# Performance work log

Measured on AMD Instinct MI355X. Metric: run time of the kernel, lower is better.

Reference implementation:

```python
import jax, jax.numpy as jnp
import numpy as np

N_NODES = 50000
N_EDGES = 400000
IN_CH = 165
HID = 64
HEADS = 8
EPS = 1e-5
NEG_SLOPE = 0.2


def _layer_norm(x, g, b):
    mu = jnp.mean(x, axis=-1, keepdims=True)
    var = jnp.mean(jnp.square(x - mu), axis=-1, keepdims=True)
    return (x - mu) * jax.lax.rsqrt(var + EPS) * g + b


def _gat_conv(x, src, dst, W, a_src, a_dst, bias, concat):
    # x: [N, F_in]; src/dst: [E] (self-loops already appended)
    N = x.shape[0]
    H, C = a_src.shape
    h = (x @ W).reshape(N, H, C)                       # [N, H, C]
    alpha_s = jnp.sum(h * a_src, axis=-1)              # [N, H]
    alpha_d = jnp.sum(h * a_dst, axis=-1)              # [N, H]
    e = jax.nn.leaky_relu(alpha_s[src] + alpha_d[dst], NEG_SLOPE)  # [E, H]
    # segment softmax over incoming edges of each dst node
    m = jax.ops.segment_max(e, dst, num_segments=N)    # [N, H]
    m = jnp.where(jnp.isfinite(m), m, 0.0)
    ex = jnp.exp(e - m[dst])                           # [E, H]
    denom = jax.ops.segment_sum(ex, dst, num_segments=N)  # [N, H]
    alpha = ex / denom[dst]                            # [E, H]
    out = jax.ops.segment_sum(alpha[:, :, None] * h[src], dst, num_segments=N)  # [N, H, C]
    if concat:
        out = out.reshape(N, H * C)
    else:
        out = out.mean(axis=1)
    return out + bias


def setup_inputs() -> dict:
    key = jax.random.key(0)
    ks = jax.random.split(key, 24)
    sc = 0.05
    d = {
        'x': jax.random.normal(ks[0], (N_NODES, IN_CH), dtype=jnp.float32),
        'edge_index': jax.random.randint(ks[1], (2, N_EDGES), 0, N_NODES, dtype=jnp.int64),
        # layer 0: in=165 -> heads*hid=512 (concat)
        'W0': jax.random.normal(ks[2], (IN_CH, HEADS * HID), jnp.float32) * sc,
        'as0': jax.random.normal(ks[3], (HEADS, HID), jnp.float32) * sc,
        'ad0': jax.random.normal(ks[4], (HEADS, HID), jnp.float32) * sc,
        'b0': jnp.zeros((HEADS * HID,), jnp.float32),
        'lng0': jnp.ones((HEADS * HID,), jnp.float32),
        'lnb0': jnp.zeros((HEADS * HID,), jnp.float32),
        # layer 1: 512 -> 512 (concat, residual applies)
        'W1': jax.random.normal(ks[5], (HEADS * HID, HEADS * HID), jnp.float32) * sc,
        'as1': jax.random.normal(ks[6], (HEADS, HID), jnp.float32) * sc,
        'ad1': jax.random.normal(ks[7], (HEADS, HID), jnp.float32) * sc,
        'b1': jnp.zeros((HEADS * HID,), jnp.float32),
        'lng1': jnp.ones((HEADS * HID,), jnp.float32),
        'lnb1': jnp.zeros((HEADS * HID,), jnp.float32),
        # layer 2: 512 -> 64 (mean over heads)
        'W2': jax.random.normal(ks[8], (HEADS * HID, HEADS * HID), jnp.float32) * sc,
        'as2': jax.random.normal(ks[9], (HEADS, HID), jnp.float32) * sc,
        'ad2': jax.random.normal(ks[10], (HEADS, HID), jnp.float32) * sc,
        'b2': jnp.zeros((HID,), jnp.float32),
        'lng2': jnp.ones((HID,), jnp.float32),
        'lnb2': jnp.zeros((HID,), jnp.float32),
        'lin_w': jax.random.normal(ks[11], (HID, 2), jnp.float32) * sc,
        'lin_b': jnp.zeros((2,), jnp.float32),
    }
    return d


def reference(x, edge_index, W0, as0, ad0, b0, lng0, lnb0,
              W1, as1, ad1, b1, lng1, lnb1,
              W2, as2, ad2, b2, lng2, lnb2, lin_w, lin_b):
    N = x.shape[0]
    loops = jnp.arange(N, dtype=edge_index.dtype)
    src = jnp.concatenate([edge_index[0], loops])
    dst = jnp.concatenate([edge_index[1], loops])

    layers = [
        (W0, as0, ad0, b0, lng0, lnb0, True),
        (W1, as1, ad1, b1, lng1, lnb1, True),
        (W2, as2, ad2, b2, lng2, lnb2, False),
    ]
    h = x
    for (W, a_s, a_d, b, g, bb, concat) in layers:
        residual = h
        h = _gat_conv(h, src, dst, W, a_s, a_d, b, concat)
        if h.shape == residual.shape:
            h = h + residual
        h = _layer_norm(h, g, bb)
        h = jax.nn.relu(h)
        # dropout is identity in eval mode
    return h @ lin_w + lin_b
```

## Files before the change

### kernel.cpp

```cpp
#include <hip/hip_runtime.h>
#include <hip/hip_bf16.h>
#include <cstdint>
#include <cstddef>

#define HEADS 8
#define HID 64
#define HF 512
#define NEG_SLOPE 0.2f
#define LN_EPS 1e-5f

typedef __hip_bfloat16 bf16;
typedef __attribute__((ext_vector_type(8))) __bf16 bf16v8;
typedef __attribute__((ext_vector_type(4))) float f32x4;

__device__ __forceinline__ float wsum64(float v) {
#pragma unroll
  for (int o = 32; o > 0; o >>= 1) v += __shfl_xor(v, o, 64);
  return v;
}
__device__ __forceinline__ int wsum64i(int v) {
#pragma unroll
  for (int o = 32; o > 0; o >>= 1) v += __shfl_xor(v, o, 64);
  return v;
}
__device__ __forceinline__ float leaky(float v) { return v >= 0.f ? v : NEG_SLOPE * v; }
__device__ __forceinline__ float bits2f(unsigned short u) {
  return __uint_as_float(((unsigned)u) << 16);
}
__device__ __forceinline__ unsigned short f2bits(float x) {
  union { bf16 h; unsigned short u; } bu;
  bu.h = __float2bfloat16(x);
  return bu.u;
}

__global__ __launch_bounds__(256)
void convert_count(const int* __restrict__ ei, int* __restrict__ esrc,
                   int* __restrict__ edst, int* __restrict__ counts, int E) {
  int e = blockIdx.x * 256 + threadIdx.x;
  if (e >= E) return;
  bool i64 = (ei[1] == 0) && (ei[3] == 0) && (ei[5] == 0) && (ei[7] == 0);
  int s, d;
  if (i64) { s = ei[2 * (size_t)e]; d = ei[2 * ((size_t)E + e)]; }
  else     { s = ei[e];             d = ei[E + e]; }
  esrc[e] = s; edst[e] = d;
  atomicAdd(&counts[d], 1);
}

#define SCAN_T 256
#define SCAN_EPT 4
#define SCAN_CHUNK (SCAN_T * SCAN_EPT)

__global__ __launch_bounds__(SCAN_T)
void scan_pass1(const int* __restrict__ counts, int* __restrict__ bsum, int N) {
  int b = blockIdx.x, t = threadIdx.x;
  int base = b * SCAN_CHUNK + t * SCAN_EPT;
  int s = 0;
#pragma unroll
  for (int i = 0; i < SCAN_EPT; ++i) {
    int idx = base + i;
    if (idx < N) s += counts[idx] + 1;
  }
  int lane = t & 63, w = t >> 6;
  int tot = wsum64i(s);
  __shared__ int ws[4];
  if (lane == 0) ws[w] = tot;
  __syncthreads();
  if (t == 0) bsum[b] = ws[0] + ws[1] + ws[2] + ws[3];
}

__global__ __launch_bounds__(64)
void scan_pass2(const int* __restrict__ bsum, int* __restrict__ boff, int NB) {
  int t = threadIdx.x;
  int own = t < NB ? bsum[t] : 0;
  int v = own;
#pragma unroll
  for (int o = 1; o < 64; o <<= 1) {
    int u = __shfl_up(v, o, 64);
    if (t >= o) v += u;
  }
  if (t < NB) boff[t] = v - own;
}

__global__ __launch_bounds__(SCAN_T)
void scan_pass3(const int* __restrict__ counts, const int* __restrict__ boff,
                int* __restrict__ row_ptr, int* __restrict__ cursor, int N, int Etot) {
  int b = blockIdx.x, t = threadIdx.x;
  int base = b * SCAN_CHUNK + t * SCAN_EPT;
  int c[SCAN_EPT];
  int s = 0;
#pragma unroll
  for (int i = 0; i < SCAN_EPT; ++i) {
    int idx = base + i;
    c[i] = idx < N ? counts[idx] + 1 : 0;
    s += c[i];
  }
  int lane = t & 63, w = t >> 6;
  int inc = s;
#pragma unroll
  for (int o = 1; o < 64; o <<= 1) {
    int u = __shfl_up(inc, o, 64);
    if (lane >= o) inc += u;
  }
  __shared__ int wsums[4];
  if (lane == 63) wsums[w] = inc;
  __syncthreads();
  int woff = 0;
  for (int i = 0; i < w; ++i) woff += wsums[i];
  int run = inc - s + woff + boff[b];
#pragma unroll
  for (int i = 0; i < SCAN_EPT; ++i) {
    int idx = base + i;
    if (idx < N) { row_ptr[idx] = run; cursor[idx] = run; run += c[i]; }
  }
  if (b == 0 && t == 0) row_ptr[N] = Etot;
}

__global__ __launch_bounds__(256)
void scatter_kernel(const int* __restrict__ esrc, const int* __restrict__ edst,
                    int* __restrict__ cursor, int* __restrict__ col, int N, int E) {
  int e = blockIdx.x * 256 + threadIdx.x;
  int Etot = E + N;
  if (e >= Etot) return;
  int s = e < E ? esrc[e] : e - E;
  int d = e < E ? edst[e] : e - E;
  int pos = atomicAdd(&cursor[d], 1);
  col[pos] = s;
}

__global__ __launch_bounds__(256)
void convert_pad_x(const float* __restrict__ x, bf16* __restrict__ xbf,
                   int M, int K, int Kp) {
  int idx = blockIdx.x * 256 + threadIdx.x;
  if (idx >= M * Kp) return;
  int row = idx / Kp, colk = idx - row * Kp;
  float v = colk < K ? x[(size_t)row * K + colk] : 0.f;
  xbf[idx] = __float2bfloat16(v);
}

__global__ __launch_bounds__(256)
void transpose_w(const float* __restrict__ W, bf16* __restrict__ Wt,
                 int K, int Ncols, int Kp) {
  int idx = blockIdx.x * 256 + threadIdx.x;
  if (idx >= Ncols * Kp) return;
  int n = idx / Kp, k = idx - n * Kp;
  float v = k < K ? W[(size_t)k * Ncols + n] : 0.f;
  Wt[idx] = __float2bfloat16(v);
}

#define LDSW 40
__global__ __launch_bounds__(256)
void gemm_mfma(const bf16* __restrict__ A, const bf16* __restrict__ Bt,
               bf16* __restrict__ C,
               const float* __restrict__ as_g, const float* __restrict__ ad_g,
               float* __restrict__ alpha_s, float* __restrict__ alpha_d,
               int M, int Ncols, int K) {
  __shared__ short Alds[128 * LDSW];
  __shared__ short Blds[128 * LDSW];
  const int tid = threadIdx.x;
  const int wave = tid >> 6, lane = tid & 63;
  const int wr = wave >> 1, wc = wave & 1;
  const int row0 = blockIdx.x * 128, col0 = blockIdx.y * 128;
  const int lrow = lane & 15;
  const int kc = lane >> 4;
  f32x4 acc[4][4] = {};

  for (int k0 = 0; k0 < K; k0 += 32) {
#pragma unroll
    for (int i = 0; i < 2; ++i) {
      int idx = tid + i * 256;
      int r = idx >> 2, c4 = idx & 3;
      uint4 va = make_uint4(0, 0, 0, 0);
      int gm = row0 + r;
      if (gm < M) va = *reinterpret_cast<const uint4*>(A + (size_t)gm * K + k0 + c4 * 8);
      *reinterpret_cast<uint4*>(&Alds[r * LDSW + c4 * 8]) = va;
      uint4 vb = *reinterpret_cast<const uint4*>(Bt + (size_t)(col0 + r) * K + k0 + c4 * 8);
      *reinterpret_cast<uint4*>(&Blds[r * LDSW + c4 * 8]) = vb;
    }
    __syncthreads();
    bf16v8 af[4], bfr[4];
#pragma unroll
    for (int r = 0; r < 4; ++r)
      af[r] = *reinterpret_cast<const bf16v8*>(&Alds[(wr * 64 + r * 16 + lrow) * LDSW + kc * 8]);
#pragma unroll
    for (int c = 0; c < 4; ++c)
      bfr[c] = *reinterpret_cast<const bf16v8*>(&Blds[(wc * 64 + c * 16 + lrow) * LDSW + kc * 8]);
#pragma unroll
    for (int r = 0; r < 4; ++r)
#pragma unroll
      for (int c = 0; c < 4; ++c)
        acc[r][c] = __builtin_amdgcn_mfma_f32_16x16x32_bf16(af[r], bfr[c], acc[r][c], 0, 0, 0);
    __syncthreads();
  }

  const int crow = (lane >> 4) * 4;
  const int ccol = lane & 15;
#pragma unroll
  for (int r = 0; r < 4; ++r) {
#pragma unroll
    for (int c = 0; c < 4; ++c) {
      int gc = col0 + wc * 64 + c * 16 + ccol;
#pragma unroll
      for (int j = 0; j < 4; ++j) {
        int gr = row0 + wr * 64 + r * 16 + crow + j;
        if (gr < M) C[(size_t)gr * Ncols + gc] = __float2bfloat16(acc[r][c][j]);
      }
    }
  }

  const int head = (col0 + wc * 64) >> 6;
  float asf[4], adf[4];
#pragma unroll
  for (int c = 0; c < 4; ++c) {
    asf[c] = as_g[head * HID + c * 16 + ccol];
    adf[c] = ad_g[head * HID + c * 16 + ccol];
  }
#pragma unroll
  for (int r = 0; r < 4; ++r) {
#pragma unroll
    for (int j = 0; j < 4; ++j) {
      float ps = 0.f, pd = 0.f;
#pragma unroll
      for (int c = 0; c < 4; ++c) {
        ps = fmaf(acc[r][c][j], asf[c], ps);
        pd = fmaf(acc[r][c][j], adf[c], pd);
      }
#pragma unroll
      for (int o = 1; o < 16; o <<= 1) {
        ps += __shfl_xor(ps, o, 64);
        pd += __shfl_xor(pd, o, 64);
      }
      if (ccol == 0) {
        int gr = row0 + wr * 64 + r * 16 + crow + j;
        if (gr < M) {
          alpha_s[gr * HEADS + head] = ps;
          alpha_d[gr * HEADS + head] = pd;
        }
      }
    }
  }
}

template <int LAYER>
__global__ __launch_bounds__(256)
void aggregate_kernel(const int* __restrict__ row_ptr, const int* __restrict__ col,
                      const bf16* __restrict__ hbuf,
                      const float* __restrict__ alpha_s, const float* __restrict__ alpha_d,
                      const bf16* __restrict__ resid,
                      const float* __restrict__ bias, const float* __restrict__ g,
                      const float* __restrict__ b,
                      bf16* __restrict__ out_bf, int N) {
  int w = threadIdx.x >> 6;
  int lane = threadIdx.x & 63;
  int nn = blockIdx.x * 4 + w;
  bool valid = nn < N;
  int n = valid ? nn : 0;
  int h = lane >> 3;
  float adh = alpha_d[n * HEADS + h];
  float m = -1e30f, den = 0.f;
  float a[8] = {};
  int lo = row_ptr[n], hi = row_ptr[n + 1];

  int sj = col[lo];
  float asj = alpha_s[sj * HEADS + h];
  uint4 u = *reinterpret_cast<const uint4*>(hbuf + (size_t)sj * HF + lane * 8);

  for (int j = lo; j < hi; ++j) {
    float e = leaky(asj + adh);
    uint4 uc = u;
    if (j + 1 < hi) {
      int sn = col[j + 1];
      asj = alpha_s[sn * HEADS + h];
      u = *reinterpret_cast<const uint4*>(hbuf + (size_t)sn * HF + lane * 8);
    }
    if (e > m) {
      float sc = __expf(m - e);
      den *= sc;
#pragma unroll
      for (int i = 0; i < 8; ++i) a[i] *= sc;
      m = e;
    }
    float ex = __expf(e - m);
    den += ex;
    const unsigned short* us = reinterpret_cast<const unsigned short*>(&uc);
#pragma unroll
    for (int i = 0; i < 8; ++i) a[i] = fmaf(ex, bits2f(us[i]), a[i]);
  }
  float inv = 1.f / den;
#pragma unroll
  for (int i = 0; i < 8; ++i) a[i] *= inv;

  if (LAYER < 2) {
    float4 b0 = ((const float4*)bias)[lane * 2];
    float4 b1 = ((const float4*)bias)[lane * 2 + 1];
    a[0] += b0.x; a[1] += b0.y; a[2] += b0.z; a[3] += b0.w;
    a[4] += b1.x; a[5] += b1.y; a[6] += b1.z; a[7] += b1.w;
    if (LAYER == 1) {
      uint4 rr = *reinterpret_cast<const uint4*>(resid + (size_t)n * HF + lane * 8);
      const unsigned short* rs = reinterpret_cast<const unsigned short*>(&rr);
#pragma unroll
      for (int i = 0; i < 8; ++i) a[i] += bits2f(rs[i]);
    }
    float s = 0.f, ss = 0.f;
#pragma unroll
    for (int i = 0; i < 8; ++i) { s += a[i]; ss += a[i] * a[i]; }
    s = wsum64(s); ss = wsum64(ss);
    float mu = s * (1.f / HF);
    float var = ss * (1.f / HF) - mu * mu;
    float rs = rsqrtf(var + LN_EPS);
    float4 g0 = ((const float4*)g)[lane * 2], g1 = ((const float4*)g)[lane * 2 + 1];
    float4 e0 = ((const float4*)b)[lane * 2], e1 = ((const float4*)b)[lane * 2 + 1];
    float gg[8] = {g0.x, g0.y, g0.z, g0.w, g1.x, g1.y, g1.z, g1.w};
    float be[8] = {e0.x, e0.y, e0.z, e0.w, e1.x, e1.y, e1.z, e1.w};
    unsigned short o[8];
#pragma unroll
    for (int i = 0; i < 8; ++i)
      o[i] = f2bits(fmaxf((a[i] - mu) * rs * gg[i] + be[i], 0.f));
    if (valid)
      *reinterpret_cast<uint4*>(out_bf + (size_t)n * HF + lane * 8) =
          *reinterpret_cast<const uint4*>(o);
  } else {
    __shared__ float lds[4][HF];
#pragma unroll
    for (int i = 0; i < 8; ++i) lds[w][lane * 8 + i] = a[i];
    float v = 0.f;
#pragma unroll
    for (int hh = 0; hh < HEADS; ++hh) v += lds[w][hh * HID + lane];
    v = v * (1.f / HEADS) + bias[lane];
    float s = wsum64(v);
    float ss = wsum64(v * v);
    float mu = s * (1.f / HID);
    float var = ss * (1.f / HID) - mu * mu;
    float rs = rsqrtf(var + LN_EPS);
    v = fmaxf((v - mu) * rs * g[lane] + b[lane], 0.f);
    if (valid) out_bf[(size_t)n * HID + lane] = __float2bfloat16(v);
  }
}

__global__ __launch_bounds__(256)
void final_linear_kernel(const bf16* __restrict__ D, const float* __restrict__ w,
                         const float* __restrict__ bb, float* __restrict__ out, int N) {
  int wid = (blockIdx.x * 256 + threadIdx.x) >> 6;
  int lane = threadIdx.x & 63;
  if (wid >= N) return;
  float v = __bfloat162float(D[(size_t)wid * HID + lane]);
  float s0 = wsum64(v * w[lane * 2 + 0]);
  float s1 = wsum64(v * w[lane * 2 + 1]);
  if (lane == 0) {
    out[(size_t)wid * 2 + 0] = s0 + bb[0];
    out[(size_t)wid * 2 + 1] = s1 + bb[1];
  }
}

extern "C" void kernel_launch(void* const* d_in, const int* in_sizes, int n_in,
                              void* d_out, int out_size, void* d_ws, size_t ws_size,
                              hipStream_t stream) {
  const float* x  = (const float*)d_in[0];
  const int*   ei = (const int*)d_in[1];
  const int N = in_sizes[0] / 165;
  const int E = in_sizes[1] / 2;
  const int Etot = E + N;
  const int K0P = 192;

  const float* W[3]  = {(const float*)d_in[2],  (const float*)d_in[8],  (const float*)d_in[14]};
  const float* As[3] = {(const float*)d_in[3],  (const float*)d_in[9],  (const float*)d_in[15]};
  const float* Ad[3] = {(const float*)d_in[4],  (const float*)d_in[10], (const float*)d_in[16]};
  const float* Bi[3] = {(const float*)d_in[5],  (const float*)d_in[11], (const float*)d_in[17]};
  const float* Lg[3] = {(const float*)d_in[6],  (const float*)d_in[12], (const float*)d_in[18]};
  const float* Lb[3] = {(const float*)d_in[7],  (const float*)d_in[13], (const float*)d_in[19]};
  const float* lin_w = (const float*)d_in[20];
  const float* lin_b = (const float*)d_in[21];

  char* p = (char*)d_ws;
  auto alloc = [&](size_t bytes) {
    char* r = p;
    p += (bytes + 255) & ~(size_t)255;
    return r;
  };
  bf16* feat0   = (bf16*)alloc((size_t)N * HF * 2);
  bf16* hbuf    = (bf16*)alloc((size_t)N * HF * 2);
  bf16* bufD    = (bf16*)alloc((size_t)N * HID * 2);
  float* alpha_s = (float*)alloc((size_t)N * HEADS * 4);
  float* alpha_d = (float*)alloc((size_t)N * HEADS * 4);
  bf16* W0t = (bf16*)alloc((size_t)HF * K0P * 2);
  bf16* W1t = (bf16*)alloc((size_t)HF * HF * 2);
  bf16* W2t = (bf16*)alloc((size_t)HF * HF * 2);
  int* esrc    = (int*)alloc((size_t)E * 4);
  int* edst    = (int*)alloc((size_t)E * 4);
  int* counts  = (int*)alloc((size_t)N * 4);
  int* row_ptr = (int*)alloc((size_t)(N + 1) * 4);
  int* cursor  = (int*)alloc((size_t)N * 4);
  int* col     = (int*)alloc((size_t)Etot * 4);
  int* bsum    = (int*)alloc((size_t)256 * 4);
  int* boff    = (int*)alloc((size_t)256 * 4);
  (void)ws_size;

  bf16* xbf = feat0;

  const int NB = (N + SCAN_CHUNK - 1) / SCAN_CHUNK;

  hipMemsetAsync(counts, 0, (size_t)N * 4, stream);
  convert_count<<<(E + 255) / 256, 256, 0, stream>>>(ei, esrc, edst, counts, E);
  scan_pass1<<<NB, SCAN_T, 0, stream>>>(counts, bsum, N);
  scan_pass2<<<1, 64, 0, stream>>>(bsum, boff, NB);
  scan_pass3<<<NB, SCAN_T, 0, stream>>>(counts, boff, row_ptr, cursor, N, Etot);
  scatter_kernel<<<(Etot + 255) / 256, 256, 0, stream>>>(esrc, edst, cursor, col, N, E);

  convert_pad_x<<<((N * K0P) + 255) / 256, 256, 0, stream>>>(x, xbf, N, 165, K0P);
  transpose_w<<<((HF * K0P) + 255) / 256, 256, 0, stream>>>(W[0], W0t, 165, HF, K0P);
  transpose_w<<<((HF * HF) + 255) / 256, 256, 0, stream>>>(W[1], W1t, HF, HF, HF);
  transpose_w<<<((HF * HF) + 255) / 256, 256, 0, stream>>>(W[2], W2t, HF, HF, HF);

  dim3 ggrid((N + 127) / 128, HF / 128);
  const int aggBlocks  = (N + 3) / 4;
  const int waveBlocks = (N + 3) / 4;

  gemm_mfma<<<ggrid, 256, 0, stream>>>(xbf, W0t, hbuf, As[0], Ad[0],
                                       alpha_s, alpha_d, N, HF, K0P);
  aggregate_kernel<0><<<aggBlocks, 256, 0, stream>>>(row_ptr, col, hbuf, alpha_s, alpha_d,
                                                     nullptr, Bi[0], Lg[0], Lb[0], feat0, N);

  gemm_mfma<<<ggrid, 256, 0, stream>>>(feat0, W1t, hbuf, As[1], Ad[1],
                                       alpha_s, alpha_d, N, HF, HF);
  aggregate_kernel<1><<<aggBlocks, 256, 0, stream>>>(row_ptr, col, hbuf, alpha_s, alpha_d,
                                                     feat0, Bi[1], Lg[1], Lb[1], feat0, N);

  gemm_mfma<<<ggrid, 256, 0, stream>>>(feat0, W2t, hbuf, As[2], Ad[2],
                                       alpha_s, alpha_d, N, HF, HF);
  aggregate_kernel<2><<<aggBlocks, 256, 0, stream>>>(row_ptr, col, hbuf, alpha_s, alpha_d,
                                                     nullptr, Bi[2], Lg[2], Lb[2], bufD, N);

  final_linear_kernel<<<waveBlocks, 256, 0, stream>>>(bufD, lin_w, lin_b, (float*)d_out, N);
}
```

Measured before the change: 516.4 us.

## Use direct global-to-LDS loads with XOR swizzle in GEMM; batch 4 edges in aggregation

The GEMM tile loads now use global_load_lds to write straight into LDS, skipping the register round trip. The LDS layout drops its padding and uses an XOR swizzle to avoid bank conflicts. The aggregation kernel now gathers four neighbours per iteration, so more independent global loads are in flight, and it does one online-softmax rescale per group of four. Tail edges are padded with a repeat of the first neighbour and masked with zero weight, which adds some redundant loads for nodes of small degree.

```diff
diff --git a/kernel.cpp b/kernel.cpp
--- a/kernel.cpp
+++ b/kernel.cpp
@@ -31,6 +31,11 @@
   union { bf16 h; unsigned short u; } bu;
   bu.h = __float2bfloat16(x);
   return bu.u;
+}
+__device__ __forceinline__ void gload_lds16(const bf16* src, short* lds_base) {
+  __builtin_amdgcn_global_load_lds(
+      (const __attribute__((address_space(1))) unsigned int*)src,
+      (__attribute__((address_space(3))) unsigned int*)lds_base, 16, 0, 0);
 }
 
 __global__ __launch_bounds__(256)
@@ -147,43 +152,47 @@
   Wt[idx] = __float2bfloat16(v);
 }
 
-#define LDSW 40
 __global__ __launch_bounds__(256)
 void gemm_mfma(const bf16* __restrict__ A, const bf16* __restrict__ Bt,
                bf16* __restrict__ C,
                const float* __restrict__ as_g, const float* __restrict__ ad_g,
                float* __restrict__ alpha_s, float* __restrict__ alpha_d,
                int M, int Ncols, int K) {
-  __shared__ short Alds[128 * LDSW];
-  __shared__ short Blds[128 * LDSW];
+  __shared__ short Alds[128 * 32];
+  __shared__ short Blds[128 * 32];
   const int tid = threadIdx.x;
   const int wave = tid >> 6, lane = tid & 63;
   const int wr = wave >> 1, wc = wave & 1;
   const int row0 = blockIdx.x * 128, col0 = blockIdx.y * 128;
   const int lrow = lane & 15;
   const int kc = lane >> 4;
+  const int sr = lane >> 2, sc4 = lane & 3;
   f32x4 acc[4][4] = {};
 
   for (int k0 = 0; k0 < K; k0 += 32) {
 #pragma unroll
     for (int i = 0; i < 2; ++i) {
-      int idx = tid + i * 256;
-      int r = idx >> 2, c4 = idx & 3;
-      uint4 va = make_uint4(0, 0, 0, 0);
-      int gm = row0 + r;
-      if (gm < M) va = *reinterpret_cast<const uint4*>(A + (size_t)gm * K + k0 + c4 * 8);
-      *reinterpret_cast<uint4*>(&Alds[r * LDSW + c4 * 8]) = va;
-      uint4 vb = *reinterpret_cast<const uint4*>(Bt + (size_t)(col0 + r) * K + k0 + c4 * 8);
-      *reinterpret_cast<uint4*>(&Blds[r * LDSW + c4 * 8]) = vb;
+      int rbase = (wave + i * 4) * 16;
+      int r = rbase + sr;
+      int slot = sc4 ^ ((r >> 1) & 3);
+      int gm = row0 + r; if (gm >= M) gm = M - 1;
+      gload_lds16(A + (size_t)gm * K + k0 + slot * 8, &Alds[rbase * 32]);
+      gload_lds16(Bt + (size_t)(col0 + r) * K + k0 + slot * 8, &Blds[rbase * 32]);
     }
     __syncthreads();
     bf16v8 af[4], bfr[4];
 #pragma unroll
-    for (int r = 0; r < 4; ++r)
-      af[r] = *reinterpret_cast<const bf16v8*>(&Alds[(wr * 64 + r * 16 + lrow) * LDSW + kc * 8]);
-#pragma unroll
-    for (int c = 0; c < 4; ++c)
-      bfr[c] = *reinterpret_cast<const bf16v8*>(&Blds[(wc * 64 + c * 16 + lrow) * LDSW + kc * 8]);
+    for (int r = 0; r < 4; ++r) {
+      int row = wr * 64 + r * 16 + lrow;
+      af[r] = *reinterpret_cast<const bf16v8*>(
+          &Alds[row * 32 + ((kc ^ ((row >> 1) & 3)) << 3)]);
+    }
+#pragma unroll
+    for (int c = 0; c < 4; ++c) {
+      int row = wc * 64 + c * 16 + lrow;
+      bfr[c] = *reinterpret_cast<const bf16v8*>(
+          &Blds[row * 32 + ((kc ^ ((row >> 1) & 3)) << 3)]);
+    }
 #pragma unroll
     for (int r = 0; r < 4; ++r)
 #pragma unroll
@@ -260,30 +269,47 @@
   float a[8] = {};
   int lo = row_ptr[n], hi = row_ptr[n + 1];
 
-  int sj = col[lo];
-  float asj = alpha_s[sj * HEADS + h];
-  uint4 u = *reinterpret_cast<const uint4*>(hbuf + (size_t)sj * HF + lane * 8);
-
-  for (int j = lo; j < hi; ++j) {
-    float e = leaky(asj + adh);
-    uint4 uc = u;
-    if (j + 1 < hi) {
-      int sn = col[j + 1];
-      asj = alpha_s[sn * HEADS + h];
-      u = *reinterpret_cast<const uint4*>(hbuf + (size_t)sn * HF + lane * 8);
-    }
-    if (e > m) {
-      float sc = __expf(m - e);
+  for (int j = lo; j < hi; j += 4) {
+    int nrem = hi - j;
+    int s0 = col[j];
+    int s1 = col[nrem > 1 ? j + 1 : lo];
+    int s2 = col[nrem > 2 ? j + 2 : lo];
+    int s3 = col[nrem > 3 ? j + 3 : lo];
+    float as0 = alpha_s[s0 * HEADS + h];
+    float as1 = alpha_s[s1 * HEADS + h];
+    float as2 = alpha_s[s2 * HEADS + h];
+    float as3 = alpha_s[s3 * HEADS + h];
+    uint4 u0 = *reinterpret_cast<const uint4*>(hbuf + (size_t)s0 * HF + lane * 8);
+    uint4 u1 = *reinterpret_cast<const uint4*>(hbuf + (size_t)s1 * HF + lane * 8);
+    uint4 u2 = *reinterpret_cast<const uint4*>(hbuf + (size_t)s2 * HF + lane * 8);
+    uint4 u3 = *reinterpret_cast<const uint4*>(hbuf + (size_t)s3 * HF + lane * 8);
+    float e0 = leaky(as0 + adh);
+    float e1 = nrem > 1 ? leaky(as1 + adh) : -1e30f;
+    float e2 = nrem > 2 ? leaky(as2 + adh) : -1e30f;
+    float e3 = nrem > 3 ? leaky(as3 + adh) : -1e30f;
+    float gmx = fmaxf(fmaxf(e0, e1), fmaxf(e2, e3));
+    if (gmx > m) {
+      float sc = __expf(m - gmx);
       den *= sc;
 #pragma unroll
       for (int i = 0; i < 8; ++i) a[i] *= sc;
-      m = e;
-    }
-    float ex = __expf(e - m);
-    den += ex;
-    const unsigned short* us = reinterpret_cast<const unsigned short*>(&uc);
-#pragma unroll
-    for (int i = 0; i < 8; ++i) a[i] = fmaf(ex, bits2f(us[i]), a[i]);
+      m = gmx;
+    }
+    float x0 = __expf(e0 - m);
+    float x1 = nrem > 1 ? __expf(e1 - m) : 0.f;
+    float x2 = nrem > 2 ? __expf(e2 - m) : 0.f;
+    float x3 = nrem > 3 ? __expf(e3 - m) : 0.f;
+    den += (x0 + x1) + (x2 + x3);
+    const unsigned short* p0 = reinterpret_cast<const unsigned short*>(&u0);
+    const unsigned short* p1 = reinterpret_cast<const unsigned short*>(&u1);
+    const unsigned short* p2 = reinterpret_cast<const unsigned short*>(&u2);
+    const unsigned short* p3 = reinterpret_cast<const unsigned short*>(&u3);
+#pragma unroll
+    for (int i = 0; i < 8; ++i) {
+      float t = fmaf(x0, bits2f(p0[i]), fmaf(x1, bits2f(p1[i]),
+                fmaf(x2, bits2f(p2[i]), x3 * bits2f(p3[i]))));
+      a[i] += t;
+    }
   }
   float inv = 1.f / den;
 #pragma unroll
```

New measurement: 477.0 us. 7.6% less time.
